# Performance work log

Hardware: AMD Instinct MI355X
Metric: run time of the kernel (lower is better)

Reference implementation:

```python
import jax, jax.numpy as jnp
import numpy as np

IN_DIM = 2
HID = 256
OUT_DIM = 1
B = 131072


def setup_inputs() -> dict:
    key = jax.random.key(0)
    ks = jax.random.split(key, 9)
    def glorot(k, shape):
        fan_in = shape[0]
        return jax.random.normal(k, shape, dtype=jnp.float32) / jnp.sqrt(jnp.float32(fan_in))
    return {
        "x": jax.random.normal(ks[0], (B, IN_DIM), dtype=jnp.float32),
        "W1": glorot(ks[1], (IN_DIM, HID)), "b1": jnp.zeros((HID,), jnp.float32),
        "W2": glorot(ks[2], (HID, HID)),    "b2": jnp.zeros((HID,), jnp.float32),
        "W3": glorot(ks[3], (HID, HID)),    "b3": jnp.zeros((HID,), jnp.float32),
        "W4": glorot(ks[4], (HID, OUT_DIM)),"b4": jnp.zeros((OUT_DIM,), jnp.float32),
    }


def reference(x, W1, b1, W2, b2, W3, b3, W4, b4):
    # Inner PINN model: tanh MLP, per-sample fn (IN_DIM,) -> (OUT_DIM,)
    def f(xi):
        h = jnp.tanh(xi @ W1 + b1)
        h = jnp.tanh(h @ W2 + b2)
        h = jnp.tanh(h @ W3 + b3)
        return h @ W4 + b4

    # Original layer computes full batch_jacobian then slices column 0.
    # Mathematically this is the directional derivative along e0, computed
    # here directly with forward-mode JVPs (same values, no wasted columns).
    e0 = jnp.zeros((IN_DIM,), x.dtype).at[0].set(1.0)

    def du_dx0(xi):  # (OUT_DIM,) : d u / d x[0]
        return jax.jvp(f, (xi,), (e0,))[1]

    def per_point(xi):
        u = f(xi)                                   # (OUT_DIM,)
        du, d2u = jax.jvp(du_dx0, (xi,), (e0,))     # du/dx0, d2u/dx0^2
        return u, du, d2u

    return jax.vmap(per_point)(x)  # each (B, OUT_DIM)
```

## Files before the change

### kernel.cpp

```cpp
#include <hip/hip_runtime.h>


#define HID 256
#define TM  32

typedef _Float16 half8 __attribute__((ext_vector_type(8)));
typedef _Float16 half4 __attribute__((ext_vector_type(4)));
typedef float    f32x4 __attribute__((ext_vector_type(4)));

#define MFMA16 __builtin_amdgcn_mfma_f32_16x16x32_f16

__device__ __forceinline__ float fast_tanh(float z) {
    const float e = __expf(2.0f * z);
#if __has_builtin(__builtin_amdgcn_rcpf)
    const float r = __builtin_amdgcn_rcpf(e + 1.0f);
#else
    const float r = 1.0f / (e + 1.0f);
#endif
    return fmaf(-2.0f, r, 1.0f);
}

__global__ __launch_bounds__(256) void prep_w(const float* __restrict__ W2,
                                              const float* __restrict__ W3,
                                              _Float16* __restrict__ wsf) {
    const int t = blockIdx.x * 256 + threadIdx.x;
    const float* __restrict__ W = (t >> 14) ? W3 : W2;
    _Float16* __restrict__ dst = wsf + (size_t)(t >> 14) * 65536;
    const int r    = t & 16383;
    const int row  = r >> 6;
    const int col0 = (r & 63) << 2;
    const f32x4 v = *(const f32x4*)&W[(size_t)row * HID + col0];
    const int kc = row >> 5;
    const int hi = (row >> 3) & 3;
    const int j  = row & 7;
    #pragma unroll
    for (int c = 0; c < 4; ++c) {
        const int col   = col0 + c;
        const int strip = col >> 4;
        const int ml    = col & 15;
        dst[((size_t)((kc * 16 + strip) * 64 + hi * 16 + ml) << 3) + j] =
            (_Float16)v[c];
    }
}

__global__ __launch_bounds__(256, 2) void pinn_mfma(
    const float* __restrict__ x,
    const float* __restrict__ W1, const float* __restrict__ b1,
    const float* __restrict__ b2, const float* __restrict__ b3,
    const float* __restrict__ W4, const float* __restrict__ b4,
    const _Float16* __restrict__ wsf,
    float* __restrict__ out, int B)
{
    __shared__ __align__(16) _Float16 Ahi[3 * 32 * 256];
    __shared__ float psumW[4][3][TM];

    const int tid  = threadIdx.x;
    const int s0   = blockIdx.x * TM;
    const int lane = tid & 63;
    const int wave = tid >> 6;

    {
        const int m  = (tid & 7) | (((tid >> 3) & 3) << 3);
        const int k0 = (tid >> 5) << 5;
        const float2 xv = *(const float2*)&x[(size_t)(s0 + m) * 2];
        const float x0 = xv.x, x1 = xv.y;
        half8 vh[3][4];
        #pragma unroll
        for (int q = 0; q < 4; ++q) {
            #pragma unroll
            for (int h = 0; h < 2; ++h) {
                const int n = k0 + q * 8 + h * 4;
                const f32x4 w0 = *(const f32x4*)&W1[n];
                const f32x4 w1 = *(const f32x4*)&W1[HID + n];
                const f32x4 bb = *(const f32x4*)&b1[n];
                #pragma unroll
                for (int r = 0; r < 4; ++r) {
                    const float z  = fmaf(x0, w0[r], fmaf(x1, w1[r], bb[r]));
                    const float a  = fast_tanh(z);
                    const float sN = 1.0f - a * a;
                    const float ad  = sN * w0[r];
                    const float add = -2.0f * a * ad * w0[r];
                    vh[0][q][h * 4 + r] = (_Float16)a;
                    vh[1][q][h * 4 + r] = (_Float16)ad;
                    vh[2][q][h * 4 + r] = (_Float16)add;
                }
            }
        }
        const int rkm = m & 7;
        const int g0  = k0 >> 3;
        #pragma unroll
        for (int s = 0; s < 3; ++s)
            #pragma unroll
            for (int q = 0; q < 4; ++q)
                *(half8*)&Ahi[s * 8192 + m * 256 + (((g0 + q) ^ rkm) << 3)] = vh[s][q];
    }
    __syncthreads();

    const int ml = lane & 15;
    const int hi = lane >> 4;
    const int rk = ml & 7;
    const int u4 = hi << 2;
    const _Float16* __restrict__ Arow = &Ahi[ml * 256];

    #pragma unroll 1
    for (int layer = 0; layer < 2; ++layer) {
        const _Float16* __restrict__ Wl =
            wsf + ((size_t)layer << 16) + (wave << 11) + (lane << 3);

        f32x4 acc[3][4][2];
        #pragma unroll
        for (int s = 0; s < 3; ++s)
            #pragma unroll
            for (int nt = 0; nt < 4; ++nt)
                #pragma unroll
                for (int mt = 0; mt < 2; ++mt)
                    acc[s][nt][mt] = (f32x4){0.f, 0.f, 0.f, 0.f};

        #pragma unroll 1
        for (int kc = 0; kc < 8; ++kc) {
            const int kn = (kc < 7) ? kc + 1 : 7;
            const _Float16* __restrict__ Wk = Wl + (kn << 13);
            half8 wnxt[4];
            #pragma unroll
            for (int nt = 0; nt < 4; ++nt)
                wnxt[nt] = *(const half8*)&Wk[nt << 9];

            const _Float16* __restrict__ Ap =
                Arow + ((((kc << 2) | hi) ^ rk) << 3);
            half8 af[3][2];
            #pragma unroll
            for (int s = 0; s < 3; ++s)
                #pragma unroll
                for (int mt = 0; mt < 2; ++mt)
                    af[s][mt] = *(const half8*)&Ap[s * 8192 + mt * 4096];

            const _Float16* __restrict__ Wc = Wl + (kc << 13);
            half8 wf[4];
            #pragma unroll
            for (int nt = 0; nt < 4; ++nt)
                wf[nt] = *(const half8*)&Wc[nt << 9];

            __builtin_amdgcn_s_setprio(1);
            #pragma unroll
            for (int nt = 0; nt < 4; ++nt)
                #pragma unroll
                for (int mt = 0; mt < 2; ++mt) {
                    acc[0][nt][mt] = MFMA16(wf[nt], af[0][mt], acc[0][nt][mt], 0, 0, 0);
                    acc[1][nt][mt] = MFMA16(wf[nt], af[1][mt], acc[1][nt][mt], 0, 0, 0);
                    acc[2][nt][mt] = MFMA16(wf[nt], af[2][mt], acc[2][nt][mt], 0, 0, 0);
                }
            __builtin_amdgcn_s_setprio(0);
            (void)wnxt;
        }

        __syncthreads();

        if (layer == 0) {
            #pragma unroll
            for (int nt = 0; nt < 4; ++nt) {
                const int ub  = (wave << 6) + (nt << 4) + u4;
                const f32x4 bb = *(const f32x4*)&b2[ub];
                const int gsw = (((ub >> 3) ^ rk) << 3) + (u4 & 4);
                #pragma unroll
                for (int mt = 0; mt < 2; ++mt) {
                    half4 hv[3];
                    #pragma unroll
                    for (int r = 0; r < 4; ++r) {
                        const float z   = acc[0][nt][mt][r] + bb[r];
                        const float a   = fast_tanh(z);
                        const float sN  = 1.0f - a * a;
                        const float zd  = acc[1][nt][mt][r];
                        const float zdd = acc[2][nt][mt][r];
                        const float ad  = sN * zd;
                        const float add = fmaf(sN, zdd, -2.0f * a * ad * zd);
                        hv[0][r] = (_Float16)a;
                        hv[1][r] = (_Float16)ad;
                        hv[2][r] = (_Float16)add;
                    }
                    const int base = (mt * 16 + ml) * 256 + gsw;
                    *(half4*)&Ahi[base]         = hv[0];
                    *(half4*)&Ahi[8192  + base] = hv[1];
                    *(half4*)&Ahi[16384 + base] = hv[2];
                }
            }
            __syncthreads();
        } else {
            float pd[3][2] = {{0.f, 0.f}, {0.f, 0.f}, {0.f, 0.f}};
            #pragma unroll
            for (int nt = 0; nt < 4; ++nt) {
                const int ub = (wave << 6) + (nt << 4) + u4;
                const f32x4 bb = *(const f32x4*)&b3[ub];
                const f32x4 w4 = *(const f32x4*)&W4[ub];
                #pragma unroll
                for (int mt = 0; mt < 2; ++mt) {
                    #pragma unroll
                    for (int r = 0; r < 4; ++r) {
                        const float z   = acc[0][nt][mt][r] + bb[r];
                        const float a   = fast_tanh(z);
                        const float sN  = 1.0f - a * a;
                        const float zd  = acc[1][nt][mt][r];
                        const float zdd = acc[2][nt][mt][r];
                        const float ad  = sN * zd;
                        const float add = fmaf(sN, zdd, -2.0f * a * ad * zd);
                        pd[0][mt] = fmaf(a,   w4[r], pd[0][mt]);
                        pd[1][mt] = fmaf(ad,  w4[r], pd[1][mt]);
                        pd[2][mt] = fmaf(add, w4[r], pd[2][mt]);
                    }
                }
            }
            #pragma unroll
            for (int s = 0; s < 3; ++s)
                #pragma unroll
                for (int mt = 0; mt < 2; ++mt) {
                    pd[s][mt] += __shfl_xor(pd[s][mt], 16, 64);
                    pd[s][mt] += __shfl_xor(pd[s][mt], 32, 64);
                }
            if (lane < 16) {
                #pragma unroll
                for (int s = 0; s < 3; ++s) {
                    psumW[wave][s][lane]      = pd[s][0];
                    psumW[wave][s][16 + lane] = pd[s][1];
                }
            }
        }
    }
    __syncthreads();

    if (tid < 96) {
        const int s = tid >> 5;
        const int m = tid & 31;
        const float v = psumW[0][s][m] + psumW[1][s][m]
                      + psumW[2][s][m] + psumW[3][s][m]
                      + ((s == 0) ? b4[0] : 0.0f);
        out[(size_t)s * B + s0 + m] = v;
    }
}

extern "C" void kernel_launch(void* const* d_in, const int* in_sizes, int n_in,
                              void* d_out, int out_size, void* d_ws, size_t ws_size,
                              hipStream_t stream) {
    const float* x  = (const float*)d_in[0];
    const float* W1 = (const float*)d_in[1];
    const float* b1 = (const float*)d_in[2];
    const float* W2 = (const float*)d_in[3];
    const float* b2 = (const float*)d_in[4];
    const float* W3 = (const float*)d_in[5];
    const float* b3 = (const float*)d_in[6];
    const float* W4 = (const float*)d_in[7];
    const float* b4 = (const float*)d_in[8];
    float* out = (float*)d_out;

    const int B = in_sizes[0] / 2;

    prep_w<<<128, 256, 0, stream>>>(W2, W3, (_Float16*)d_ws);
    pinn_mfma<<<B / TM, 256, 0, stream>>>(x, W1, b1, b2, b3, W4, b4,
                                          (const _Float16*)d_ws, out, B);
}
```

Baseline: 180.3 us.

## Switch hidden-layer GEMMs from 16x16x32 to 32x32x16 MFMA tiles

Replaces the 16x16x32 f16 MFMA tiling with 32x32x16 MFMA. The weight pre-swizzle layout, LDS A-fragment addressing, accumulator layout, epilogue indexing and final cross-lane reduction are all reworked to match. Each wave now issues 6 larger MFMAs per k-step over 16 k-steps, loading fewer fragments per MFMA. The intent is to cut LDS and global fragment traffic and instruction overhead per unit of compute. The unused prefetch of next-step weights is also dropped.

```diff
diff --git a/kernel.cpp b/kernel.cpp
--- a/kernel.cpp
+++ b/kernel.cpp
@@ -4,11 +4,12 @@
 #define HID 256
 #define TM  32
 
-typedef _Float16 half8 __attribute__((ext_vector_type(8)));
-typedef _Float16 half4 __attribute__((ext_vector_type(4)));
-typedef float    f32x4 __attribute__((ext_vector_type(4)));
-
-#define MFMA16 __builtin_amdgcn_mfma_f32_16x16x32_f16
+typedef _Float16 half8  __attribute__((ext_vector_type(8)));
+typedef _Float16 half4  __attribute__((ext_vector_type(4)));
+typedef float    f32x4  __attribute__((ext_vector_type(4)));
+typedef float    f32x16 __attribute__((ext_vector_type(16)));
+
+#define MFMA32 __builtin_amdgcn_mfma_f32_32x32x16_f16
 
 __device__ __forceinline__ float fast_tanh(float z) {
     const float e = __expf(2.0f * z);
@@ -30,16 +31,15 @@
     const int row  = r >> 6;
     const int col0 = (r & 63) << 2;
     const f32x4 v = *(const f32x4*)&W[(size_t)row * HID + col0];
-    const int kc = row >> 5;
-    const int hi = (row >> 3) & 3;
-    const int j  = row & 7;
+    const int kc  = row >> 4;
+    const int sub = (row >> 3) & 1;
+    const int j   = row & 7;
     #pragma unroll
     for (int c = 0; c < 4; ++c) {
         const int col   = col0 + c;
-        const int strip = col >> 4;
-        const int ml    = col & 15;
-        dst[((size_t)((kc * 16 + strip) * 64 + hi * 16 + ml) << 3) + j] =
-            (_Float16)v[c];
+        const int strip = col >> 5;
+        const int lane  = (sub << 5) + (col & 31);
+        dst[((size_t)((kc * 8 + strip) * 64 + lane) << 3) + j] = (_Float16)v[c];
     }
 }
 
@@ -96,88 +96,71 @@
     }
     __syncthreads();
 
-    const int ml = lane & 15;
-    const int hi = lane >> 4;
-    const int rk = ml & 7;
-    const int u4 = hi << 2;
-    const _Float16* __restrict__ Arow = &Ahi[ml * 256];
+    const int ml5 = lane & 31;
+    const int hi5 = lane >> 5;
+    const int rk  = ml5 & 7;
+    const _Float16* __restrict__ Arow = &Ahi[ml5 * 256];
 
     #pragma unroll 1
     for (int layer = 0; layer < 2; ++layer) {
         const _Float16* __restrict__ Wl =
-            wsf + ((size_t)layer << 16) + (wave << 11) + (lane << 3);
-
-        f32x4 acc[3][4][2];
+            wsf + ((size_t)layer << 16) + (wave << 10) + (lane << 3);
+
+        f32x16 acc[3][2];
         #pragma unroll
         for (int s = 0; s < 3; ++s)
             #pragma unroll
-            for (int nt = 0; nt < 4; ++nt)
-                #pragma unroll
-                for (int mt = 0; mt < 2; ++mt)
-                    acc[s][nt][mt] = (f32x4){0.f, 0.f, 0.f, 0.f};
+            for (int st = 0; st < 2; ++st)
+                acc[s][st] = (f32x16){0.f,0.f,0.f,0.f,0.f,0.f,0.f,0.f,
+                                      0.f,0.f,0.f,0.f,0.f,0.f,0.f,0.f};
 
         #pragma unroll 1
-        for (int kc = 0; kc < 8; ++kc) {
-            const int kn = (kc < 7) ? kc + 1 : 7;
-            const _Float16* __restrict__ Wk = Wl + (kn << 13);
-            half8 wnxt[4];
-            #pragma unroll
-            for (int nt = 0; nt < 4; ++nt)
-                wnxt[nt] = *(const half8*)&Wk[nt << 9];
-
+        for (int kc = 0; kc < 16; ++kc) {
             const _Float16* __restrict__ Ap =
-                Arow + ((((kc << 2) | hi) ^ rk) << 3);
-            half8 af[3][2];
-            #pragma unroll
-            for (int s = 0; s < 3; ++s)
-                #pragma unroll
-                for (int mt = 0; mt < 2; ++mt)
-                    af[s][mt] = *(const half8*)&Ap[s * 8192 + mt * 4096];
-
-            const _Float16* __restrict__ Wc = Wl + (kc << 13);
-            half8 wf[4];
-            #pragma unroll
-            for (int nt = 0; nt < 4; ++nt)
-                wf[nt] = *(const half8*)&Wc[nt << 9];
+                Arow + ((((kc << 1) | hi5) ^ rk) << 3);
+            const half8 af0 = *(const half8*)&Ap[0];
+            const half8 af1 = *(const half8*)&Ap[8192];
+            const half8 af2 = *(const half8*)&Ap[16384];
+            const _Float16* __restrict__ Wk = Wl + (kc << 12);
+            const half8 wf0 = *(const half8*)&Wk[0];
+            const half8 wf1 = *(const half8*)&Wk[512];
 
             __builtin_amdgcn_s_setprio(1);
-            #pragma unroll
-            for (int nt = 0; nt < 4; ++nt)
-                #pragma unroll
-                for (int mt = 0; mt < 2; ++mt) {
-                    acc[0][nt][mt] = MFMA16(wf[nt], af[0][mt], acc[0][nt][mt], 0, 0, 0);
-                    acc[1][nt][mt] = MFMA16(wf[nt], af[1][mt], acc[1][nt][mt], 0, 0, 0);
-                    acc[2][nt][mt] = MFMA16(wf[nt], af[2][mt], acc[2][nt][mt], 0, 0, 0);
-                }
+            acc[0][0] = MFMA32(wf0, af0, acc[0][0], 0, 0, 0);
+            acc[1][0] = MFMA32(wf0, af1, acc[1][0], 0, 0, 0);
+            acc[2][0] = MFMA32(wf0, af2, acc[2][0], 0, 0, 0);
+            acc[0][1] = MFMA32(wf1, af0, acc[0][1], 0, 0, 0);
+            acc[1][1] = MFMA32(wf1, af1, acc[1][1], 0, 0, 0);
+            acc[2][1] = MFMA32(wf1, af2, acc[2][1], 0, 0, 0);
             __builtin_amdgcn_s_setprio(0);
-            (void)wnxt;
         }
 
         __syncthreads();
 
         if (layer == 0) {
             #pragma unroll
-            for (int nt = 0; nt < 4; ++nt) {
-                const int ub  = (wave << 6) + (nt << 4) + u4;
-                const f32x4 bb = *(const f32x4*)&b2[ub];
-                const int gsw = (((ub >> 3) ^ rk) << 3) + (u4 & 4);
-                #pragma unroll
-                for (int mt = 0; mt < 2; ++mt) {
+            for (int st = 0; st < 2; ++st) {
+                const int strip = (wave << 1) + st;
+                #pragma unroll
+                for (int q = 0; q < 4; ++q) {
+                    const int ub = (strip << 5) + (q << 3) + (hi5 << 2);
+                    const f32x4 bb = *(const f32x4*)&b2[ub];
                     half4 hv[3];
                     #pragma unroll
                     for (int r = 0; r < 4; ++r) {
-                        const float z   = acc[0][nt][mt][r] + bb[r];
+                        const float z   = acc[0][st][q * 4 + r] + bb[r];
                         const float a   = fast_tanh(z);
                         const float sN  = 1.0f - a * a;
-                        const float zd  = acc[1][nt][mt][r];
-                        const float zdd = acc[2][nt][mt][r];
+                        const float zd  = acc[1][st][q * 4 + r];
+                        const float zdd = acc[2][st][q * 4 + r];
                         const float ad  = sN * zd;
                         const float add = fmaf(sN, zdd, -2.0f * a * ad * zd);
                         hv[0][r] = (_Float16)a;
                         hv[1][r] = (_Float16)ad;
                         hv[2][r] = (_Float16)add;
                     }
-                    const int base = (mt * 16 + ml) * 256 + gsw;
+                    const int gsw  = ((((strip << 2) + q) ^ rk) << 3) + (hi5 << 2);
+                    const int base = ml5 * 256 + gsw;
                     *(half4*)&Ahi[base]         = hv[0];
                     *(half4*)&Ahi[8192  + base] = hv[1];
                     *(half4*)&Ahi[16384 + base] = hv[2];
@@ -185,42 +168,37 @@
             }
             __syncthreads();
         } else {
-            float pd[3][2] = {{0.f, 0.f}, {0.f, 0.f}, {0.f, 0.f}};
-            #pragma unroll
-            for (int nt = 0; nt < 4; ++nt) {
-                const int ub = (wave << 6) + (nt << 4) + u4;
-                const f32x4 bb = *(const f32x4*)&b3[ub];
-                const f32x4 w4 = *(const f32x4*)&W4[ub];
-                #pragma unroll
-                for (int mt = 0; mt < 2; ++mt) {
+            float pd[3] = {0.f, 0.f, 0.f};
+            #pragma unroll
+            for (int st = 0; st < 2; ++st) {
+                const int strip = (wave << 1) + st;
+                #pragma unroll
+                for (int q = 0; q < 4; ++q) {
+                    const int ub = (strip << 5) + (q << 3) + (hi5 << 2);
+                    const f32x4 bb = *(const f32x4*)&b3[ub];
+                    const f32x4 w4 = *(const f32x4*)&W4[ub];
                     #pragma unroll
                     for (int r = 0; r < 4; ++r) {
-                        const float z   = acc[0][nt][mt][r] + bb[r];
+                        const float z   = acc[0][st][q * 4 + r] + bb[r];
                         const float a   = fast_tanh(z);
                         const float sN  = 1.0f - a * a;
-                        const float zd  = acc[1][nt][mt][r];
-                        const float zdd = acc[2][nt][mt][r];
+                        const float zd  = acc[1][st][q * 4 + r];
+                        const float zdd = acc[2][st][q * 4 + r];
                         const float ad  = sN * zd;
                         const float add = fmaf(sN, zdd, -2.0f * a * ad * zd);
-                        pd[0][mt] = fmaf(a,   w4[r], pd[0][mt]);
-                        pd[1][mt] = fmaf(ad,  w4[r], pd[1][mt]);
-                        pd[2][mt] = fmaf(add, w4[r], pd[2][mt]);
+                        pd[0] = fmaf(a,   w4[r], pd[0]);
+                        pd[1] = fmaf(ad,  w4[r], pd[1]);
+                        pd[2] = fmaf(add, w4[r], pd[2]);
                     }
                 }
             }
             #pragma unroll
             for (int s = 0; s < 3; ++s)
-                #pragma unroll
-                for (int mt = 0; mt < 2; ++mt) {
-                    pd[s][mt] += __shfl_xor(pd[s][mt], 16, 64);
-                    pd[s][mt] += __shfl_xor(pd[s][mt], 32, 64);
-                }
-            if (lane < 16) {
-                #pragma unroll
-                for (int s = 0; s < 3; ++s) {
-                    psumW[wave][s][lane]      = pd[s][0];
-                    psumW[wave][s][16 + lane] = pd[s][1];
-                }
+                pd[s] += __shfl_xor(pd[s], 32, 64);
+            if (lane < 32) {
+                #pragma unroll
+                for (int s = 0; s < 3; ++s)
+                    psumW[wave][s][lane] = pd[s];
             }
         }
     }
```

Result: slower. 197.4 us (+9.5%).
